# Kernel optimization log

Measured on AMD Instinct MI355X. Metric: run time of the kernel, lower is better.

The kernel has to match this reference:

```python
import jax, jax.numpy as jnp
import numpy as np

K = 3
P = K // 2


def _conv(x, w, b):
    y = jax.lax.conv_general_dilated(x, w, (1, 1), [(P, P), (P, P)],
                                     dimension_numbers=('NCHW', 'OIHW', 'NCHW'))
    return y + b[None, :, None, None]


def _deform_sample(x, py, px):
    # x: [B,C,H,W]; py,px: [B,KK,H,W] float sample coords -> [B,C,KK,H,W]
    B, C, H, W = x.shape
    xf = x.reshape(B, C, H * W)
    y0 = jnp.floor(py)
    x0 = jnp.floor(px)
    wy = py - y0
    wx = px - x0

    def corner(yi, xi, w):
        valid = (yi >= 0) & (yi < H) & (xi >= 0) & (xi < W)  # zero-pad outside
        idx = (jnp.clip(yi, 0, H - 1) * W + jnp.clip(xi, 0, W - 1)).astype(jnp.int32)
        g = jax.vmap(lambda xb, ib: xb[:, ib])(xf, idx)  # [B,C,KK,H,W]
        return g * (w * valid)[:, None]

    return (corner(y0, x0, (1 - wy) * (1 - wx)) + corner(y0, x0 + 1, (1 - wy) * wx)
            + corner(y0 + 1, x0, wy * (1 - wx)) + corner(y0 + 1, x0 + 1, wy * wx))


def setup_inputs() -> dict:
    key = jax.random.key(0)
    ks = jax.random.split(key, 8)
    B, C, H, W = 4, 256, 80, 80
    x = jax.random.normal(ks[0], (B, C, H, W), dtype=jnp.float32)
    offset_w = jax.random.normal(ks[1], (2 * K * K, C, K, K), dtype=jnp.float32) * 0.01
    offset_b = jax.random.normal(ks[2], (2 * K * K,), dtype=jnp.float32) * 0.01
    dcn_w = jax.random.normal(ks[3], (C, C, K, K), dtype=jnp.float32) * (1.0 / np.sqrt(C * K * K))
    gamma = jnp.ones((C,), jnp.float32)
    beta = jnp.zeros((C,), jnp.float32)
    mean = jax.random.normal(ks[4], (C,), dtype=jnp.float32) * 0.1
    var = jax.random.uniform(ks[5], (C,), dtype=jnp.float32, minval=0.5, maxval=1.5)
    return {'x': x, 'offset_w': offset_w, 'offset_b': offset_b, 'dcn_w': dcn_w,
            'gamma': gamma, 'beta': beta, 'mean': mean, 'var': var}


def reference(x, offset_w, offset_b, dcn_w, gamma, beta, mean, var):
    B, C, H, W = x.shape
    # offset conv -> [B, KK, 2(dy,dx), H, W] (torchvision DeformConv2d layout)
    off = _conv(x, offset_w, offset_b).reshape(B, K * K, 2, H, W)
    ki = jnp.repeat(jnp.arange(K), K).astype(x.dtype)  # kernel-tap row offset
    kj = jnp.tile(jnp.arange(K), K).astype(x.dtype)    # kernel-tap col offset
    hh = jnp.arange(H, dtype=x.dtype)
    ww = jnp.arange(W, dtype=x.dtype)
    py = off[:, :, 0] + (hh - P)[None, None, :, None] + ki[None, :, None, None]
    px = off[:, :, 1] + (ww - P)[None, None, None, :] + kj[None, :, None, None]
    vals = _deform_sample(x, py, px)                      # [B,C,KK,H,W]
    y = jnp.einsum('bckhw,ock->bohw', vals, dcn_w.reshape(C, C, K * K))
    # eval-mode BatchNorm + SiLU
    inv = jax.lax.rsqrt(var + 1e-5)
    y = (y - mean[None, :, None, None]) * (gamma * inv)[None, :, None, None] + beta[None, :, None, None]
    y = y * jax.nn.sigmoid(y)
    return x + y
```

## Files before the change

kernel.cpp:

```cpp
#include <hip/hip_runtime.h>
#include <math.h>
#include <stdint.h>

#define BATCH 4
#define CH    256
#define HH    80
#define WW    80
#define HW    (HH*WW)
#define NPIX  (BATCH*HW)
#define KK    9
#define CO    18
#define NCHUNK 72
#define NIV   36
#define PXB   64
#define NBLK  (NPIX/PXB)
#define AST   72

typedef _Float16 half8 __attribute__((ext_vector_type(8)));
typedef float    f32x4 __attribute__((ext_vector_type(4)));

__global__ __launch_bounds__(256) void k_transpose_x(const float* __restrict__ x,
                                                     _Float16* __restrict__ xt) {
    __shared__ float tile[32][33];
    int b  = blockIdx.z;
    int c0 = blockIdx.y * 32;
    int p0 = blockIdx.x * 32;
    int tx = threadIdx.x;
    int ty = threadIdx.y;
    const float* xb = x + (size_t)b * CH * HW;
    #pragma unroll
    for (int i = 0; i < 32; i += 8)
        tile[ty + i][tx] = xb[(size_t)(c0 + ty + i) * HW + p0 + tx];
    __syncthreads();
    _Float16* xtb = xt + (size_t)b * HW * CH;
    #pragma unroll
    for (int i = 0; i < 32; i += 8)
        xtb[(size_t)(p0 + ty + i) * CH + c0 + tx] = (_Float16)tile[tx][ty + i];
}

__global__ __launch_bounds__(256) void k_pack_all(const float* __restrict__ w,
                                                  const float* __restrict__ ow,
                                                  _Float16* __restrict__ wp,
                                                  _Float16* __restrict__ wpo) {
    int idx = blockIdx.x * 256 + threadIdx.x;
    if (idx < NIV * 16384) {
        int e    = idx & 7;
        int lane = (idx >> 3) & 63;
        int nn   = (idx >> 9) & 1;
        int ks   = (idx >> 10) & 1;
        int og   = (idx >> 11) & 7;
        int iv   = idx >> 14;
        int oc = og * 32 + nn * 16 + (lane & 15);
        int kl = ks * 32 + (lane >> 4) * 8 + e;
        int kg = iv * 64 + kl;
        int q  = kg >> 5;
        int tap = q >> 3;
        int c   = (q & 7) * 32 + (kg & 31);
        wp[idx] = (_Float16)w[((size_t)oc * CH + c) * KK + tap];
        return;
    }
    int idx2 = idx - NIV * 16384;
    if (idx2 >= NCHUNK * 1024) return;
    int e    = idx2 & 7;
    int lane = (idx2 >> 3) & 63;
    int nf   = (idx2 >> 9) & 1;
    int q    = idx2 >> 10;
    int oc  = nf * 16 + (lane & 15);
    int kic = (lane >> 4) * 8 + e;
    int tap = q >> 3;
    int c   = (q & 7) * 32 + kic;
    float v = (oc < CO) ? ow[((size_t)oc * CH + c) * KK + tap] : 0.f;
    wpo[idx2] = (_Float16)v;
}

#define BODY(IV, IVEND, BCUR, BNXT, RBUF, WBUF)                                    \
  {                                                                                \
    __syncthreads();                                                               \
    const int iv_ = (IV);                                                          \
    half8 pre[4]; float cwa[4];                                                    \
    if (iv_ < (IVEND) - 1) {                                                       \
      const _Float16* wb = wpk4 + (size_t)(iv_ + 1) * 16384 + og * 2048 + lane * 8;\
      BNXT[0] = *(const half8*)(wb);                                               \
      BNXT[1] = *(const half8*)(wb + 512);                                         \
      BNXT[2] = *(const half8*)(wb + 1024);                                        \
      BNXT[3] = *(const half8*)(wb + 1536);                                        \
      int chunk = 2 * (iv_ + 1) + sub;                                             \
      int tap = chunk >> 3, cg = chunk & 7;                                        \
      int4 ncb = cbl[gpx][tap]; float4 ncw = cwl[gpx][tap];                        \
      pre[0] = *(const half8*)(xtb + (size_t)ncb.x + cg * 32 + ko);                \
      pre[1] = *(const half8*)(xtb + (size_t)ncb.y + cg * 32 + ko);                \
      pre[2] = *(const half8*)(xtb + (size_t)ncb.z + cg * 32 + ko);                \
      pre[3] = *(const half8*)(xtb + (size_t)ncb.w + cg * 32 + ko);                \
      cwa[0] = ncw.x; cwa[1] = ncw.y; cwa[2] = ncw.z; cwa[3] = ncw.w;              \
    }                                                                              \
    __builtin_amdgcn_s_setprio(1);                                                 \
    _Pragma("unroll")                                                              \
    for (int mm = 0; mm < 4; ++mm) {                                               \
      half8 a0 = *(const half8*)&Ab[RBUF][(mm * 16 + lm) * AST + kg8];             \
      half8 a1 = *(const half8*)&Ab[RBUF][(mm * 16 + lm) * AST + 32 + kg8];        \
      acc[mm][0] = __builtin_amdgcn_mfma_f32_16x16x32_f16(a0, BCUR[0], acc[mm][0], 0, 0, 0); \
      acc[mm][1] = __builtin_amdgcn_mfma_f32_16x16x32_f16(a0, BCUR[1], acc[mm][1], 0, 0, 0); \
      acc[mm][0] = __builtin_amdgcn_mfma_f32_16x16x32_f16(a1, BCUR[2], acc[mm][0], 0, 0, 0); \
      acc[mm][1] = __builtin_amdgcn_mfma_f32_16x16x32_f16(a1, BCUR[3], acc[mm][1], 0, 0, 0); \
    }                                                                              \
    __builtin_amdgcn_s_setprio(0);                                                 \
    if (iv_ < (IVEND) - 1) {                                                       \
      half8 v = pre[0] * (_Float16)cwa[0];                                         \
      v += pre[1] * (_Float16)cwa[1];                                              \
      v += pre[2] * (_Float16)cwa[2];                                              \
      v += pre[3] * (_Float16)cwa[3];                                              \
      *(half8*)&Ab[WBUF][gpx * AST + cq * 8] = v;                                  \
    }                                                                              \
  }

__global__ __launch_bounds__(512, 4) void k_main(const float* __restrict__ x,
                                                 const _Float16* __restrict__ xt,
                                                 const _Float16* __restrict__ wpk4,
                                                 const _Float16* __restrict__ wopf,
                                                 const float* __restrict__ obias,
                                                 const float* __restrict__ gamma,
                                                 const float* __restrict__ beta,
                                                 const float* __restrict__ mean,
                                                 const float* __restrict__ var,
                                                 float* __restrict__ out) {
    __shared__ _Float16 Ab[2][PXB * AST];
    __shared__ int4     cbl[PXB][KK];
    __shared__ float4   cwl[PXB][KK];
    __shared__ float    offl[2][PXB][CO];

    int t = threadIdx.x, lane = t & 63, og = t >> 6;
    int lm = lane & 15, kg8 = (lane >> 4) * 8;
    int tile = ((int)blockIdx.x & 7) * (NBLK / 8) + ((int)blockIdx.x >> 3);
    int pixbase = tile * PXB;
    int bb = pixbase / HW, hw0 = pixbase % HW;
    const _Float16* xtb = xt + (size_t)bb * HW * CH;

    {
        int pxf = og & 3, kh = og >> 2;
        int apx = hw0 + pxf * 16 + lm;
        int h = apx / WW, w = apx % WW;
        f32x4 oacc0 = (f32x4)0.f, oacc1 = (f32x4)0.f;
        #pragma unroll
        for (int qq = 0; qq < NCHUNK / 2; ++qq) {
            int q = kh * (NCHUNK / 2) + qq;
            int tap = q >> 3, cg = q & 7;
            int ki = tap / 3, kj = tap - ki * 3;
            int yy = h + ki - 1, xx = w + kj - 1;
            bool ok = (yy >= 0) && (yy < HH) && (xx >= 0) && (xx < WW);
            int yc = min(max(yy, 0), HH - 1), xc = min(max(xx, 0), WW - 1);
            half8 a = {0, 0, 0, 0, 0, 0, 0, 0};
            if (ok) a = *(const half8*)(xtb + (size_t)(yc * WW + xc) * CH + cg * 32 + kg8);
            const _Float16* wb = wopf + (size_t)q * 1024 + lane * 8;
            half8 b0 = *(const half8*)(wb);
            half8 b1 = *(const half8*)(wb + 512);
            oacc0 = __builtin_amdgcn_mfma_f32_16x16x32_f16(a, b0, oacc0, 0, 0, 0);
            oacc1 = __builtin_amdgcn_mfma_f32_16x16x32_f16(a, b1, oacc1, 0, 0, 0);
        }
        int prow = pxf * 16 + (lane >> 4) * 4;
        #pragma unroll
        for (int r = 0; r < 4; ++r) offl[kh][prow + r][lm] = oacc0[r];
        if (lm < CO - 16) {
            #pragma unroll
            for (int r = 0; r < 4; ++r) offl[kh][prow + r][16 + lm] = oacc1[r];
        }
    }
    __syncthreads();

    for (int task = t; task < PXB * KK; task += 512) {
        int p = task / KK, tap = task - (task / KK) * KK;
        float dy = offl[0][p][2 * tap]     + offl[1][p][2 * tap]     + obias[2 * tap];
        float dx = offl[0][p][2 * tap + 1] + offl[1][p][2 * tap + 1] + obias[2 * tap + 1];
        int hw = hw0 + p, hc = hw / WW, wc = hw % WW;
        int ki = tap / 3, kj = tap - ki * 3;
        float py = dy + (float)(hc - 1 + ki);
        float px = dx + (float)(wc - 1 + kj);
        float y0f = floorf(py), x0f = floorf(px);
        float wy = py - y0f, wx = px - x0f;
        int y0 = (int)y0f, x0 = (int)x0f;
        int cb[4]; float cw[4];
        #pragma unroll
        for (int cy = 0; cy < 2; ++cy)
            #pragma unroll
            for (int cx = 0; cx < 2; ++cx) {
                int yy = y0 + cy, xx = x0 + cx;
                bool okc = (yy >= 0) && (yy < HH) && (xx >= 0) && (xx < WW);
                int yc = min(max(yy, 0), HH - 1);
                int xc = min(max(xx, 0), WW - 1);
                float wgt = (cy ? wy : 1.f - wy) * (cx ? wx : 1.f - wx);
                cb[cy * 2 + cx] = (yc * WW + xc) * CH;
                cw[cy * 2 + cx] = okc ? wgt : 0.f;
            }
        cbl[p][tap] = make_int4(cb[0], cb[1], cb[2], cb[3]);
        cwl[p][tap] = make_float4(cw[0], cw[1], cw[2], cw[3]);
    }
    __syncthreads();

    int gpx = t >> 3, cq = t & 7;
    int sub = cq >> 2, ko = (cq & 3) * 8;

    half8 bfA[4], bfB[4];
    {
        const _Float16* wb = wpk4 + og * 2048 + lane * 8;
        bfA[0] = *(const half8*)(wb);
        bfA[1] = *(const half8*)(wb + 512);
        bfA[2] = *(const half8*)(wb + 1024);
        bfA[3] = *(const half8*)(wb + 1536);
    }
    {
        int4 cb = cbl[gpx][0];
        float4 cw = cwl[gpx][0];
        int cg = sub;
        half8 v = *(const half8*)(xtb + (size_t)cb.x + cg * 32 + ko) * (_Float16)cw.x;
        v += *(const half8*)(xtb + (size_t)cb.y + cg * 32 + ko) * (_Float16)cw.y;
        v += *(const half8*)(xtb + (size_t)cb.z + cg * 32 + ko) * (_Float16)cw.z;
        v += *(const half8*)(xtb + (size_t)cb.w + cg * 32 + ko) * (_Float16)cw.w;
        *(half8*)&Ab[0][gpx * AST + cq * 8] = v;
    }

    f32x4 acc[4][2];
    #pragma unroll
    for (int mm = 0; mm < 4; ++mm) {
        acc[mm][0] = (f32x4)0.f;
        acc[mm][1] = (f32x4)0.f;
    }

    for (int ii = 0; ii < NIV; ii += 2) {
        BODY(ii,     NIV, bfA, bfB, 0, 1)
        BODY(ii + 1, NIV, bfB, bfA, 1, 0)
    }

    const float* xb2  = x   + (size_t)bb * CH * HW;
    float*       outb = out + (size_t)bb * CH * HW;
    #pragma unroll
    for (int nn = 0; nn < 2; ++nn) {
        int oc = og * 32 + nn * 16 + lm;
        float sc = gamma[oc] * rsqrtf(var[oc] + 1e-5f);
        float mn = mean[oc], bt = beta[oc];
        const float* xr   = xb2  + (size_t)oc * HW + hw0;
        float*       orow = outb + (size_t)oc * HW + hw0;
        #pragma unroll
        for (int mm = 0; mm < 4; ++mm) {
            int pb2 = mm * 16 + (lane >> 4) * 4;
            #pragma unroll
            for (int r = 0; r < 4; ++r) {
                float yv = (acc[mm][nn][r] - mn) * sc + bt;
                float s = yv * __builtin_amdgcn_rcpf(1.f + __expf(-yv));
                orow[pb2 + r] = xr[pb2 + r] + s;
            }
        }
    }
}

extern "C" void kernel_launch(void* const* d_in, const int* in_sizes, int n_in,
                              void* d_out, int out_size, void* d_ws, size_t ws_size,
                              hipStream_t stream) {
    const float* x        = (const float*)d_in[0];
    const float* offset_w = (const float*)d_in[1];
    const float* offset_b = (const float*)d_in[2];
    const float* dcn_w    = (const float*)d_in[3];
    const float* gamma    = (const float*)d_in[4];
    const float* beta     = (const float*)d_in[5];
    const float* mean     = (const float*)d_in[6];
    const float* var      = (const float*)d_in[7];
    float* out = (float*)d_out;

    _Float16* xt   = (_Float16*)d_ws;
    _Float16* wpk4 = xt + (size_t)NPIX * CH;
    _Float16* wopf = wpk4 + (size_t)NIV * 16384;

    k_transpose_x<<<dim3(HW / 32, CH / 32, BATCH), dim3(32, 8), 0, stream>>>(x, xt);
    k_pack_all<<<(NIV * 16384 + NCHUNK * 1024 + 255) / 256, 256, 0, stream>>>(dcn_w, offset_w, wpk4, wopf);
    k_main<<<NBLK, 512, 0, stream>>>(x, xt, wpk4, wopf, offset_b,
                                     gamma, beta, mean, var, out);
}
```

Measured before the change: 91.92 us.

## Double pixel tile to 128, software-pipeline offset conv, alias shared memory

Raises the per-block pixel tile from 64 to 128, so each wave keeps 8x2 MFMA accumulators and every loaded weight fragment is reused over twice as many pixels. The offset-conv prologue now runs all 72 chunks per wave with an 8-deep software-pipelined load queue instead of splitting the K range across two wave halves and summing partials. Shared buffers are packed into one aliased pool so the larger tile fits, and occupancy is lowered to 2 blocks per CU. The aim is less weight-load traffic and better latency hiding, at the cost of more registers, fewer resident waves and half as many blocks.

New measurement: 95.14 us. 1.03x slower.

```diff
diff --git a/kernel.cpp b/kernel.cpp
--- a/kernel.cpp
+++ b/kernel.cpp
@@ -12,7 +12,7 @@
 #define CO    18
 #define NCHUNK 72
 #define NIV   36
-#define PXB   64
+#define PXB   128
 #define NBLK  (NPIX/PXB)
 #define AST   72
 
@@ -73,47 +73,74 @@
     wpo[idx2] = (_Float16)v;
 }
 
-#define BODY(IV, IVEND, BCUR, BNXT, RBUF, WBUF)                                    \
-  {                                                                                \
-    __syncthreads();                                                               \
-    const int iv_ = (IV);                                                          \
-    half8 pre[4]; float cwa[4];                                                    \
-    if (iv_ < (IVEND) - 1) {                                                       \
-      const _Float16* wb = wpk4 + (size_t)(iv_ + 1) * 16384 + og * 2048 + lane * 8;\
-      BNXT[0] = *(const half8*)(wb);                                               \
-      BNXT[1] = *(const half8*)(wb + 512);                                         \
-      BNXT[2] = *(const half8*)(wb + 1024);                                        \
-      BNXT[3] = *(const half8*)(wb + 1536);                                        \
-      int chunk = 2 * (iv_ + 1) + sub;                                             \
-      int tap = chunk >> 3, cg = chunk & 7;                                        \
-      int4 ncb = cbl[gpx][tap]; float4 ncw = cwl[gpx][tap];                        \
-      pre[0] = *(const half8*)(xtb + (size_t)ncb.x + cg * 32 + ko);                \
-      pre[1] = *(const half8*)(xtb + (size_t)ncb.y + cg * 32 + ko);                \
-      pre[2] = *(const half8*)(xtb + (size_t)ncb.z + cg * 32 + ko);                \
-      pre[3] = *(const half8*)(xtb + (size_t)ncb.w + cg * 32 + ko);                \
-      cwa[0] = ncw.x; cwa[1] = ncw.y; cwa[2] = ncw.z; cwa[3] = ncw.w;              \
-    }                                                                              \
-    __builtin_amdgcn_s_setprio(1);                                                 \
-    _Pragma("unroll")                                                              \
-    for (int mm = 0; mm < 4; ++mm) {                                               \
-      half8 a0 = *(const half8*)&Ab[RBUF][(mm * 16 + lm) * AST + kg8];             \
-      half8 a1 = *(const half8*)&Ab[RBUF][(mm * 16 + lm) * AST + 32 + kg8];        \
+#define P1L(S, Q)                                                                   \
+  { int q_ = (Q);                                                                   \
+    if (q_ < NCHUNK) {                                                              \
+      int tap_ = q_ >> 3, cg_ = q_ & 7;                                             \
+      int ki_ = tap_ / 3, kj_ = tap_ - ki_ * 3;                                     \
+      int yy_ = h + ki_ - 1, xx_ = w + kj_ - 1;                                     \
+      bool ok_ = (yy_ >= 0) && (yy_ < HH) && (xx_ >= 0) && (xx_ < WW);              \
+      pa##S = (half8){0, 0, 0, 0, 0, 0, 0, 0};                                      \
+      if (ok_) pa##S = *(const half8*)(xtb + (size_t)(yy_ * WW + xx_) * CH + cg_ * 32 + kg8); \
+      const _Float16* wq_ = wopf + (size_t)q_ * 1024 + lane * 8;                    \
+      pb##S = *(const half8*)(wq_);                                                 \
+      pc##S = *(const half8*)(wq_ + 512);                                           \
+    } }
+#define P1M(S)                                                                      \
+  o0 = __builtin_amdgcn_mfma_f32_16x16x32_f16(pa##S, pb##S, o0, 0, 0, 0);           \
+  o1 = __builtin_amdgcn_mfma_f32_16x16x32_f16(pa##S, pc##S, o1, 0, 0, 0);
+
+#define BODY(IV, BCUR, BNXT, ABR, ABW)                                              \
+  {                                                                                 \
+    __syncthreads();                                                                \
+    const int iv_ = (IV);                                                           \
+    half8 pre[2][4]; float cwa[2][4];                                               \
+    if (iv_ < NIV - 1) {                                                            \
+      const _Float16* wb = wpk4 + (size_t)(iv_ + 1) * 16384 + og * 2048 + lane * 8; \
+      BNXT[0] = *(const half8*)(wb);                                                \
+      BNXT[1] = *(const half8*)(wb + 512);                                          \
+      BNXT[2] = *(const half8*)(wb + 1024);                                         \
+      BNXT[3] = *(const half8*)(wb + 1536);                                         \
+      _Pragma("unroll")                                                             \
+      for (int s = 0; s < 2; ++s) {                                                 \
+        int qd = sl + 4 * s;                                                        \
+        int sub_ = qd >> 2, ko_ = (qd & 3) * 8;                                     \
+        int chunk = 2 * (iv_ + 1) + sub_;                                           \
+        int tap_ = chunk >> 3, cg_ = chunk & 7;                                     \
+        int4 ncb = cbl[gpx * KK + tap_];                                            \
+        float4 ncw = cwl[gpx * KK + tap_];                                          \
+        pre[s][0] = *(const half8*)(xtb + (size_t)ncb.x + cg_ * 32 + ko_);          \
+        pre[s][1] = *(const half8*)(xtb + (size_t)ncb.y + cg_ * 32 + ko_);          \
+        pre[s][2] = *(const half8*)(xtb + (size_t)ncb.z + cg_ * 32 + ko_);          \
+        pre[s][3] = *(const half8*)(xtb + (size_t)ncb.w + cg_ * 32 + ko_);          \
+        cwa[s][0] = ncw.x; cwa[s][1] = ncw.y; cwa[s][2] = ncw.z; cwa[s][3] = ncw.w; \
+      }                                                                             \
+    }                                                                               \
+    __builtin_amdgcn_s_setprio(1);                                                  \
+    _Pragma("unroll")                                                               \
+    for (int mm = 0; mm < 8; ++mm) {                                                \
+      half8 a0 = *(const half8*)&ABR[(mm * 16 + lm) * AST + kg8];                   \
+      half8 a1 = *(const half8*)&ABR[(mm * 16 + lm) * AST + 32 + kg8];              \
       acc[mm][0] = __builtin_amdgcn_mfma_f32_16x16x32_f16(a0, BCUR[0], acc[mm][0], 0, 0, 0); \
       acc[mm][1] = __builtin_amdgcn_mfma_f32_16x16x32_f16(a0, BCUR[1], acc[mm][1], 0, 0, 0); \
       acc[mm][0] = __builtin_amdgcn_mfma_f32_16x16x32_f16(a1, BCUR[2], acc[mm][0], 0, 0, 0); \
       acc[mm][1] = __builtin_amdgcn_mfma_f32_16x16x32_f16(a1, BCUR[3], acc[mm][1], 0, 0, 0); \
-    }                                                                              \
-    __builtin_amdgcn_s_setprio(0);                                                 \
-    if (iv_ < (IVEND) - 1) {                                                       \
-      half8 v = pre[0] * (_Float16)cwa[0];                                         \
-      v += pre[1] * (_Float16)cwa[1];                                              \
-      v += pre[2] * (_Float16)cwa[2];                                              \
-      v += pre[3] * (_Float16)cwa[3];                                              \
-      *(half8*)&Ab[WBUF][gpx * AST + cq * 8] = v;                                  \
-    }                                                                              \
+    }                                                                               \
+    __builtin_amdgcn_s_setprio(0);                                                  \
+    if (iv_ < NIV - 1) {                                                            \
+      _Pragma("unroll")                                                             \
+      for (int s = 0; s < 2; ++s) {                                                 \
+        int qd = sl + 4 * s;                                                        \
+        half8 v = pre[s][0] * (_Float16)cwa[s][0];                                  \
+        v += pre[s][1] * (_Float16)cwa[s][1];                                       \
+        v += pre[s][2] * (_Float16)cwa[s][2];                                       \
+        v += pre[s][3] * (_Float16)cwa[s][3];                                       \
+        *(half8*)&ABW[gpx * AST + qd * 8] = v;                                      \
+      }                                                                             \
+    }                                                                               \
   }
 
-__global__ __launch_bounds__(512, 4) void k_main(const float* __restrict__ x,
+__global__ __launch_bounds__(512, 2) void k_main(const float* __restrict__ x,
                                                  const _Float16* __restrict__ xt,
                                                  const _Float16* __restrict__ wpk4,
                                                  const _Float16* __restrict__ wopf,
@@ -123,10 +150,12 @@
                                                  const float* __restrict__ mean,
                                                  const float* __restrict__ var,
                                                  float* __restrict__ out) {
-    __shared__ _Float16 Ab[2][PXB * AST];
-    __shared__ int4     cbl[PXB][KK];
-    __shared__ float4   cwl[PXB][KK];
-    __shared__ float    offl[2][PXB][CO];
+    __shared__ __align__(16) char pool[73728];
+    _Float16* Ab0 = (_Float16*)pool;
+    _Float16* Ab1 = (_Float16*)(pool + 18432);
+    int4*     cbl = (int4*)(pool + 36864);
+    float4*   cwl = (float4*)(pool + 55296);
+    float*    offl = (float*)pool;
 
     int t = threadIdx.x, lane = t & 63, og = t >> 6;
     int lm = lane & 15, kg8 = (lane >> 4) * 8;
@@ -136,40 +165,38 @@
     const _Float16* xtb = xt + (size_t)bb * HW * CH;
 
     {
-        int pxf = og & 3, kh = og >> 2;
-        int apx = hw0 + pxf * 16 + lm;
+        int apx = hw0 + og * 16 + lm;
         int h = apx / WW, w = apx % WW;
-        f32x4 oacc0 = (f32x4)0.f, oacc1 = (f32x4)0.f;
+        f32x4 o0 = (f32x4)0.f, o1 = (f32x4)0.f;
+        half8 pa0, pa1, pa2, pa3, pa4, pa5, pa6, pa7;
+        half8 pb0, pb1, pb2, pb3, pb4, pb5, pb6, pb7;
+        half8 pc0, pc1, pc2, pc3, pc4, pc5, pc6, pc7;
+        P1L(0, 0) P1L(1, 1) P1L(2, 2) P1L(3, 3)
+        P1L(4, 4) P1L(5, 5) P1L(6, 6) P1L(7, 7)
+        for (int q = 0; q < NCHUNK; q += 8) {
+            P1M(0) P1L(0, q + 8)
+            P1M(1) P1L(1, q + 9)
+            P1M(2) P1L(2, q + 10)
+            P1M(3) P1L(3, q + 11)
+            P1M(4) P1L(4, q + 12)
+            P1M(5) P1L(5, q + 13)
+            P1M(6) P1L(6, q + 14)
+            P1M(7) P1L(7, q + 15)
+        }
+        int prow = og * 16 + (lane >> 4) * 4;
         #pragma unroll
-        for (int qq = 0; qq < NCHUNK / 2; ++qq) {
-            int q = kh * (NCHUNK / 2) + qq;
-            int tap = q >> 3, cg = q & 7;
-            int ki = tap / 3, kj = tap - ki * 3;
-            int yy = h + ki - 1, xx = w + kj - 1;
-            bool ok = (yy >= 0) && (yy < HH) && (xx >= 0) && (xx < WW);
-            int yc = min(max(yy, 0), HH - 1), xc = min(max(xx, 0), WW - 1);
-            half8 a = {0, 0, 0, 0, 0, 0, 0, 0};
-            if (ok) a = *(const half8*)(xtb + (size_t)(yc * WW + xc) * CH + cg * 32 + kg8);
-            const _Float16* wb = wopf + (size_t)q * 1024 + lane * 8;
-            half8 b0 = *(const half8*)(wb);
-            half8 b1 = *(const half8*)(wb + 512);
-            oacc0 = __builtin_amdgcn_mfma_f32_16x16x32_f16(a, b0, oacc0, 0, 0, 0);
-            oacc1 = __builtin_amdgcn_mfma_f32_16x16x32_f16(a, b1, oacc1, 0, 0, 0);
-        }
-        int prow = pxf * 16 + (lane >> 4) * 4;
-        #pragma unroll
-        for (int r = 0; r < 4; ++r) offl[kh][prow + r][lm] = oacc0[r];
+        for (int r = 0; r < 4; ++r) offl[(prow + r) * CO + lm] = o0[r];
         if (lm < CO - 16) {
             #pragma unroll
-            for (int r = 0; r < 4; ++r) offl[kh][prow + r][16 + lm] = oacc1[r];
+            for (int r = 0; r < 4; ++r) offl[(prow + r) * CO + 16 + lm] = o1[r];
         }
     }
     __syncthreads();
 
     for (int task = t; task < PXB * KK; task += 512) {
         int p = task / KK, tap = task - (task / KK) * KK;
-        float dy = offl[0][p][2 * tap]     + offl[1][p][2 * tap]     + obias[2 * tap];
-        float dx = offl[0][p][2 * tap + 1] + offl[1][p][2 * tap + 1] + obias[2 * tap + 1];
+        float dy = offl[p * CO + 2 * tap]     + obias[2 * tap];
+        float dx = offl[p * CO + 2 * tap + 1] + obias[2 * tap + 1];
         int hw = hw0 + p, hc = hw / WW, wc = hw % WW;
         int ki = tap / 3, kj = tap - ki * 3;
         float py = dy + (float)(hc - 1 + ki);
@@ -190,13 +217,12 @@
                 cb[cy * 2 + cx] = (yc * WW + xc) * CH;
                 cw[cy * 2 + cx] = okc ? wgt : 0.f;
             }
-        cbl[p][tap] = make_int4(cb[0], cb[1], cb[2], cb[3]);
-        cwl[p][tap] = make_float4(cw[0], cw[1], cw[2], cw[3]);
+        cbl[task] = make_int4(cb[0], cb[1], cb[2], cb[3]);
+        cwl[task] = make_float4(cw[0], cw[1], cw[2], cw[3]);
     }
     __syncthreads();
 
-    int gpx = t >> 3, cq = t & 7;
-    int sub = cq >> 2, ko = (cq & 3) * 8;
+    int gpx = t >> 2, sl = t & 3;
 
     half8 bfA[4], bfB[4];
     {
@@ -207,26 +233,30 @@
         bfA[3] = *(const half8*)(wb + 1536);
     }
     {
-        int4 cb = cbl[gpx][0];
-        float4 cw = cwl[gpx][0];
-        int cg = sub;
-        half8 v = *(const half8*)(xtb + (size_t)cb.x + cg * 32 + ko) * (_Float16)cw.x;
-        v += *(const half8*)(xtb + (size_t)cb.y + cg * 32 + ko) * (_Float16)cw.y;
-        v += *(const half8*)(xtb + (size_t)cb.z + cg * 32 + ko) * (_Float16)cw.z;
-        v += *(const half8*)(xtb + (size_t)cb.w + cg * 32 + ko) * (_Float16)cw.w;
-        *(half8*)&Ab[0][gpx * AST + cq * 8] = v;
-    }
-
-    f32x4 acc[4][2];
+        int4 cb = cbl[gpx * KK];
+        float4 cw = cwl[gpx * KK];
+        #pragma unroll
+        for (int s = 0; s < 2; ++s) {
+            int qd = sl + 4 * s;
+            int cg = qd >> 2, ko = (qd & 3) * 8;
+            half8 v = *(const half8*)(xtb + (size_t)cb.x + cg * 32 + ko) * (_Float16)cw.x;
+            v += *(const half8*)(xtb + (size_t)cb.y + cg * 32 + ko) * (_Float16)cw.y;
+            v += *(const half8*)(xtb + (size_t)cb.z + cg * 32 + ko) * (_Float16)cw.z;
+            v += *(const half8*)(xtb + (size_t)cb.w + cg * 32 + ko) * (_Float16)cw.w;
+            *(half8*)&Ab0[gpx * AST + qd * 8] = v;
+        }
+    }
+
+    f32x4 acc[8][2];
     #pragma unroll
-    for (int mm = 0; mm < 4; ++mm) {
+    for (int mm = 0; mm < 8; ++mm) {
         acc[mm][0] = (f32x4)0.f;
         acc[mm][1] = (f32x4)0.f;
     }
 
     for (int ii = 0; ii < NIV; ii += 2) {
-        BODY(ii,     NIV, bfA, bfB, 0, 1)
-        BODY(ii + 1, NIV, bfB, bfA, 1, 0)
+        BODY(ii,     bfA, bfB, Ab0, Ab1)
+        BODY(ii + 1, bfB, bfA, Ab1, Ab0)
     }
 
     const float* xb2  = x   + (size_t)bb * CH * HW;
@@ -239,7 +269,7 @@
         const float* xr   = xb2  + (size_t)oc * HW + hw0;
         float*       orow = outb + (size_t)oc * HW + hw0;
         #pragma unroll
-        for (int mm = 0; mm < 4; ++mm) {
+        for (int mm = 0; mm < 8; ++mm) {
             int pb2 = mm * 16 + (lane >> 4) * 4;
             #pragma unroll
             for (int r = 0; r < 4; ++r) {
```

## Split offset-conv reduction four ways with two pixel tiles per wave, alias LDS

Applied to the files above, without the earlier changes.

The offset-convolution prologue now gives each wave two 16-pixel tiles and a quarter of the K reduction (18 chunks) instead of one tile and half the reduction. Each loaded weight fragment then feeds two MFMAs, which halves weight-load traffic and shortens the serial chain per wave. The four partial sums are reduced when the offsets are read. Shared memory is merged into one aliased pool, with offl overlaying the Ab buffer, to keep LDS use down and preserve occupancy. The risks are higher register pressure and a possible hazard if Ab is written before offl has been fully consumed.

New measurement: 88.84 us. 1.03x faster.

```diff
diff --git a/kernel.cpp b/kernel.cpp
--- a/kernel.cpp
+++ b/kernel.cpp
@@ -123,10 +123,11 @@
                                                  const float* __restrict__ mean,
                                                  const float* __restrict__ var,
                                                  float* __restrict__ out) {
-    __shared__ _Float16 Ab[2][PXB * AST];
-    __shared__ int4     cbl[PXB][KK];
-    __shared__ float4   cwl[PXB][KK];
-    __shared__ float    offl[2][PXB][CO];
+    __shared__ __align__(16) char pool[46080];
+    _Float16 (*Ab)[PXB * AST] = (_Float16 (*)[PXB * AST])pool;
+    int4   (*cbl)[KK] = (int4 (*)[KK])(pool + 18432);
+    float4 (*cwl)[KK] = (float4 (*)[KK])(pool + 27648);
+    float*  offl      = (float*)pool;
 
     int t = threadIdx.x, lane = t & 63, og = t >> 6;
     int lm = lane & 15, kg8 = (lane >> 4) * 8;
@@ -136,40 +137,61 @@
     const _Float16* xtb = xt + (size_t)bb * HW * CH;
 
     {
-        int pxf = og & 3, kh = og >> 2;
-        int apx = hw0 + pxf * 16 + lm;
-        int h = apx / WW, w = apx % WW;
-        f32x4 oacc0 = (f32x4)0.f, oacc1 = (f32x4)0.f;
-        #pragma unroll
-        for (int qq = 0; qq < NCHUNK / 2; ++qq) {
-            int q = kh * (NCHUNK / 2) + qq;
+        int pxh = og & 1;
+        int kq  = og >> 1;
+        int apx0 = hw0 + pxh * 32 + lm;
+        int apx1 = apx0 + 16;
+        int h0 = apx0 / WW, w0 = apx0 % WW;
+        int h1 = apx1 / WW, w1 = apx1 % WW;
+        f32x4 oa0 = (f32x4)0.f, oa1 = (f32x4)0.f;
+        f32x4 ob0 = (f32x4)0.f, ob1 = (f32x4)0.f;
+        #pragma unroll
+        for (int qq = 0; qq < 18; ++qq) {
+            int q = kq * 18 + qq;
             int tap = q >> 3, cg = q & 7;
             int ki = tap / 3, kj = tap - ki * 3;
-            int yy = h + ki - 1, xx = w + kj - 1;
-            bool ok = (yy >= 0) && (yy < HH) && (xx >= 0) && (xx < WW);
-            int yc = min(max(yy, 0), HH - 1), xc = min(max(xx, 0), WW - 1);
-            half8 a = {0, 0, 0, 0, 0, 0, 0, 0};
-            if (ok) a = *(const half8*)(xtb + (size_t)(yc * WW + xc) * CH + cg * 32 + kg8);
-            const _Float16* wb = wopf + (size_t)q * 1024 + lane * 8;
-            half8 b0 = *(const half8*)(wb);
-            half8 b1 = *(const half8*)(wb + 512);
-            oacc0 = __builtin_amdgcn_mfma_f32_16x16x32_f16(a, b0, oacc0, 0, 0, 0);
-            oacc1 = __builtin_amdgcn_mfma_f32_16x16x32_f16(a, b1, oacc1, 0, 0, 0);
-        }
-        int prow = pxf * 16 + (lane >> 4) * 4;
-        #pragma unroll
-        for (int r = 0; r < 4; ++r) offl[kh][prow + r][lm] = oacc0[r];
+            int yy0 = h0 + ki - 1, xx0 = w0 + kj - 1;
+            int yy1 = h1 + ki - 1, xx1 = w1 + kj - 1;
+            bool ok0 = (yy0 >= 0) && (yy0 < HH) && (xx0 >= 0) && (xx0 < WW);
+            bool ok1 = (yy1 >= 0) && (yy1 < HH) && (xx1 >= 0) && (xx1 < WW);
+            half8 a0 = {0, 0, 0, 0, 0, 0, 0, 0};
+            half8 a1 = {0, 0, 0, 0, 0, 0, 0, 0};
+            if (ok0) a0 = *(const half8*)(xtb + (size_t)(yy0 * WW + xx0) * CH + cg * 32 + kg8);
+            if (ok1) a1 = *(const half8*)(xtb + (size_t)(yy1 * WW + xx1) * CH + cg * 32 + kg8);
+            const _Float16* wq = wopf + (size_t)q * 1024 + lane * 8;
+            half8 b0 = *(const half8*)(wq);
+            half8 b1 = *(const half8*)(wq + 512);
+            oa0 = __builtin_amdgcn_mfma_f32_16x16x32_f16(a0, b0, oa0, 0, 0, 0);
+            oa1 = __builtin_amdgcn_mfma_f32_16x16x32_f16(a0, b1, oa1, 0, 0, 0);
+            ob0 = __builtin_amdgcn_mfma_f32_16x16x32_f16(a1, b0, ob0, 0, 0, 0);
+            ob1 = __builtin_amdgcn_mfma_f32_16x16x32_f16(a1, b1, ob1, 0, 0, 0);
+        }
+        int prow = (lane >> 4) * 4;
+        int r0 = (kq * PXB) + pxh * 32 + prow;
+        int r1 = r0 + 16;
+        #pragma unroll
+        for (int r = 0; r < 4; ++r) {
+            offl[(r0 + r) * CO + lm] = oa0[r];
+            offl[(r1 + r) * CO + lm] = ob0[r];
+        }
         if (lm < CO - 16) {
             #pragma unroll
-            for (int r = 0; r < 4; ++r) offl[kh][prow + r][16 + lm] = oacc1[r];
+            for (int r = 0; r < 4; ++r) {
+                offl[(r0 + r) * CO + 16 + lm] = oa1[r];
+                offl[(r1 + r) * CO + 16 + lm] = ob1[r];
+            }
         }
     }
     __syncthreads();
 
     for (int task = t; task < PXB * KK; task += 512) {
         int p = task / KK, tap = task - (task / KK) * KK;
-        float dy = offl[0][p][2 * tap]     + offl[1][p][2 * tap]     + obias[2 * tap];
-        float dx = offl[0][p][2 * tap + 1] + offl[1][p][2 * tap + 1] + obias[2 * tap + 1];
+        float dy = obias[2 * tap], dx = obias[2 * tap + 1];
+        #pragma unroll
+        for (int ks = 0; ks < 4; ++ks) {
+            dy += offl[((ks * PXB) + p) * CO + 2 * tap];
+            dx += offl[((ks * PXB) + p) * CO + 2 * tap + 1];
+        }
         int hw = hw0 + p, hc = hw / WW, wc = hw % WW;
         int ki = tap / 3, kj = tap - ki * 3;
         float py = dy + (float)(hc - 1 + ki);
```
